# Performance work log

Measured on AMD Instinct MI355X. Metric: run time of the kernel, lower is better.

The kernel has to match this reference:

```python
import jax, jax.numpy as jnp
import numpy as np

N, E, R, D, L, B, K = 50000, 800000, 64, 64, 4, 2, 32


def setup_inputs() -> dict:
    ks = jax.random.split(jax.random.key(0), 10)
    return {
        "edge_index": jax.random.randint(ks[0], (2, E), 0, N),
        "edge_type": jax.random.randint(ks[1], (E,), 0, R),
        "h_index": jax.random.randint(ks[2], (B,), 0, N),
        "r_index": jax.random.randint(ks[3], (B,), 0, R),
        "t_index": jax.random.randint(ks[4], (B, K), 0, N),
        "rel_repr": jax.random.normal(ks[5], (B, R, D)) * 0.1,
        "boundary_extra": jax.random.normal(ks[6], (B, N, D)) * 0.02,
        "layers_W": jax.random.normal(ks[7], (L, 2 * D, D)) / np.sqrt(2 * D),
        "layers_b": jnp.zeros((L, D)),
        "ln_g": jnp.ones((L, D)),
        "ln_b": jnp.zeros((L, D)),
        "w1": jax.random.normal(ks[8], (2 * D, D)) / np.sqrt(2 * D),
        "b1": jnp.zeros((D,)),
        "w2": jax.random.normal(ks[9], (D,)) / np.sqrt(D),
        "b2": jnp.zeros((1,)),
    }


def _layer_norm(x, g, b, eps=1e-5):
    mu = x.mean(-1, keepdims=True)
    var = ((x - mu) ** 2).mean(-1, keepdims=True)
    return (x - mu) * jax.lax.rsqrt(var + eps) * g + b


def reference(edge_index, edge_type, h_index, r_index, t_index, rel_repr,
              boundary_extra, layers_W, layers_b, ln_g, ln_b, w1, b1, w2, b2):
    src, dst = edge_index[0], edge_index[1]
    query = rel_repr[jnp.arange(B), r_index]  # [B, D] per-query relation embedding
    # enhanced boundary: entity/relation-enhanced base + query injected at head node
    boundary = boundary_extra.at[jnp.arange(B), h_index].add(query)  # [B, N, D]
    seg = jax.vmap(lambda m: jax.ops.segment_sum(m, dst, num_segments=N))
    x = boundary
    for l in range(L):
        msg = x[:, src, :] * rel_repr[:, edge_type, :]   # DistMult messages [B, E, D]
        agg = seg(msg) + boundary                        # sum aggregation + boundary self-message
        out = jnp.einsum('bnd,df->bnf', jnp.concatenate([x, agg], -1), layers_W[l]) + layers_b[l]
        out = jax.nn.relu(_layer_norm(out, ln_g[l], ln_b[l]))
        x = out + x                                      # short_cut residual
    node_feat = jnp.concatenate(
        [x, jnp.broadcast_to(query[:, None, :], (B, N, D))], axis=-1)  # [B, N, 2D]
    feat = node_feat[jnp.arange(B)[:, None], t_index]    # gather tails [B, K, 2D]
    h = jax.nn.relu(feat @ w1 + b1)
    score = h @ w2 + b2                                  # [B, K]
    return score
```

## Files before the change

kernel.cpp:

```cpp
#include <hip/hip_runtime.h>
#include <hip/hip_bf16.h>

#define NN 50000
#define EE 800000
#define RR 64
#define DD 64
#define LL 4
#define BB 2
#define KK 32

#define NBUK 98
#define BROWS 512
#define CHUNK 2048
#define NBLK 391
#define PLACE_CAP 10240
#define CAP3 8192

#define PREP_BLKS 196
#define INIT_BLKS 3125
#define HIST_BLKS 391

#define PB_REL   0
#define PB_WT    8192
#define PB_LB    40960
#define PB_G     41216
#define PB_BETA  41472
#define PB_W1    41728
#define PB_B1    49920
#define PB_W2    49984
#define PB_B2    50048
#define PB_TOT   50049

typedef short v8s __attribute__((ext_vector_type(8)));
typedef float v4f __attribute__((ext_vector_type(4)));
typedef _Float16 v2h __attribute__((ext_vector_type(2)));
typedef _Float16 v4h __attribute__((ext_vector_type(4)));
typedef _Float16 v8h __attribute__((ext_vector_type(8)));
typedef unsigned short v4u __attribute__((ext_vector_type(4)));

static __device__ __forceinline__ float ldany(const void* p, int i, int flag) {
    if (flag) return __bfloat162float(((const __hip_bfloat16*)p)[i]);
    return ((const float*)p)[i];
}
static __device__ __forceinline__ unsigned short tobf(float x) {
    return (unsigned short)(__builtin_bit_cast(unsigned int, x) >> 16);
}
static __device__ __forceinline__ unsigned short rnebf(float x) {
    unsigned int u = __builtin_bit_cast(unsigned int, x);
    return (unsigned short)((u + 0x7FFFu + ((u >> 16) & 1u)) >> 16);
}
static __device__ __forceinline__ float frombf(unsigned short h) {
    return __builtin_bit_cast(float, ((unsigned int)h) << 16);
}
static __device__ __forceinline__ int getflag(const unsigned int* lng) {
    return (*lng == 0x3F803F80u) ? 1 : 0;
}

__global__ void __launch_bounds__(256) k_prep(const void* __restrict__ rel, const void* __restrict__ lb,
                       const void* __restrict__ g, const void* __restrict__ beta,
                       const void* __restrict__ w1, const void* __restrict__ b1,
                       const void* __restrict__ w2, const void* __restrict__ b2,
                       const void* __restrict__ W, const unsigned int* __restrict__ lng,
                       const void* __restrict__ be,
                       const int* __restrict__ h_index, const int* __restrict__ r_index,
                       const int* __restrict__ ei,
                       float* __restrict__ pb, unsigned short* __restrict__ wshi,
                       unsigned short* __restrict__ wslo, _Float16* __restrict__ relH,
                       _Float16* __restrict__ xH, int* __restrict__ bucketCount) {
    __shared__ int h[NBUK];
    int blk = blockIdx.x, t = threadIdx.x;
    int flag = getflag(lng);

    if (blk >= PREP_BLKS + INIT_BLKS) {
        if (t < NBUK) h[t] = 0;
        __syncthreads();
        int base = (blk - PREP_BLKS - INIT_BLKS) * CHUNK;
        #pragma unroll
        for (int i = 0; i < 8; ++i) {
            int e = base + i * 256 + t;
            if (e < EE) atomicAdd(&h[ei[EE + e] >> 9], 1);
        }
        __syncthreads();
        if (t < NBUK && h[t]) atomicAdd(&bucketCount[t], h[t]);
        return;
    }
    if (blk >= PREP_BLKS) {
        int gid = (blk - PREP_BLKS) * 256 + t;
        int n = gid >> 4, j = gid & 15, d0 = j * 4;
        float x0[4], x1[4];
        if (flag) {
            v4u a = *(const v4u*)((const unsigned short*)be + (size_t)n * 64 + d0);
            v4u bq = *(const v4u*)((const unsigned short*)be + (size_t)(NN + n) * 64 + d0);
            #pragma unroll
            for (int jj = 0; jj < 4; ++jj) { x0[jj] = frombf(a[jj]); x1[jj] = frombf(bq[jj]); }
        } else {
            v4f a = *(const v4f*)((const float*)be + (size_t)n * 64 + d0);
            v4f bq = *(const v4f*)((const float*)be + (size_t)(NN + n) * 64 + d0);
            #pragma unroll
            for (int jj = 0; jj < 4; ++jj) { x0[jj] = a[jj]; x1[jj] = bq[jj]; }
        }
        if (n == h_index[0]) {
            int r = r_index[0];
            #pragma unroll
            for (int jj = 0; jj < 4; ++jj) x0[jj] += ldany(rel, r * DD + d0 + jj, flag);
        }
        if (n == h_index[1]) {
            int r = r_index[1];
            #pragma unroll
            for (int jj = 0; jj < 4; ++jj) x1[jj] += ldany(rel, (RR + r) * DD + d0 + jj, flag);
        }
        v8h o;
        #pragma unroll
        for (int jj = 0; jj < 4; ++jj) {
            o[2 * jj]     = (_Float16)x0[jj];
            o[2 * jj + 1] = (_Float16)x1[jj];
        }
        *(v8h*)(xH + (size_t)n * 128 + d0 * 2) = o;
        return;
    }

    int gid = blk * 256 + t;
    if (gid < 32768) {
        int l = gid >> 13, r = gid & 8191, f = r >> 7, d = r & 127;
        float w = ldany(W, l * 8192 + d * 64 + f, flag);
        unsigned short h2 = tobf(w);
        wshi[gid] = h2;
        wslo[gid] = tobf(w - frombf(h2));
        if (gid < 8192) {
            int ty = gid >> 7, rr = gid & 127, dd = rr >> 1, b = rr & 1;
            relH[gid] = (_Float16)ldany(rel, b * 4096 + ty * 64 + dd, flag);
        }
    }
    if (gid >= PB_TOT) return;
    if (gid < PB_WT) { pb[gid] = ldany(rel, gid, flag); return; }
    if (gid < PB_LB) return;
    if (gid < PB_G)    { pb[gid] = ldany(lb,   gid - PB_LB,   flag); return; }
    if (gid < PB_BETA) { pb[gid] = ldany(g,    gid - PB_G,    flag); return; }
    if (gid < PB_W1)   { pb[gid] = ldany(beta, gid - PB_BETA, flag); return; }
    if (gid < PB_B1)   { pb[gid] = ldany(w1,   gid - PB_W1,   flag); return; }
    if (gid < PB_W2)   { pb[gid] = ldany(b1,   gid - PB_B1,   flag); return; }
    if (gid < PB_B2)   { pb[gid] = ldany(w2,   gid - PB_W2,   flag); return; }
    pb[gid] = ldany(b2, 0, flag);
}

__global__ void __launch_bounds__(256) k_bfill(const int* __restrict__ ei,
                                               const int* __restrict__ et,
                                               const int* __restrict__ bucketCount,
                                               int* __restrict__ bcur,
                                               unsigned int* __restrict__ btmp) {
    __shared__ int h[NBUK], rb[NBUK], sb[128];
    int t = threadIdx.x;
    int v = 0;
    if (t < 128) { v = (t < NBUK) ? bucketCount[t] : 0; sb[t] = v; }
    __syncthreads();
    for (int off = 1; off < 128; off <<= 1) {
        int a = (t < 128 && t >= off) ? sb[t - off] : 0;
        __syncthreads();
        if (t < 128 && t >= off) sb[t] += a;
        __syncthreads();
    }
    if (t < NBUK) sb[t] -= v;
    if (t < NBUK) h[t] = 0;
    __syncthreads();
    int base = blockIdx.x * CHUNK;
    unsigned int rec[8]; int bk[8];
    #pragma unroll
    for (int i = 0; i < 8; ++i) {
        int e = base + i * 256 + t;
        bk[i] = -1;
        if (e < EE) {
            int dst = ei[EE + e];
            rec[i] = (unsigned int)ei[e] | ((unsigned int)et[e] << 16)
                   | ((unsigned int)(dst & 511) << 22);
            bk[i] = dst >> 9;
            atomicAdd(&h[bk[i]], 1);
        }
    }
    __syncthreads();
    if (t < NBUK) rb[t] = h[t] ? (sb[t] + atomicAdd(&bcur[t], h[t])) : 0;
    __syncthreads();
    if (t < NBUK) h[t] = 0;
    __syncthreads();
    #pragma unroll
    for (int i = 0; i < 8; ++i) {
        if (bk[i] >= 0) {
            int pos = rb[bk[i]] + atomicAdd(&h[bk[i]], 1);
            btmp[pos] = rec[i];
        }
    }
}

__global__ void __launch_bounds__(256) k_place(const int* __restrict__ bucketCount,
                                               const unsigned int* __restrict__ btmp,
                                               unsigned int* __restrict__ elist,
                                               int* __restrict__ rowptr) {
    __shared__ int rp[BROWS + 1];
    __shared__ int cur[BROWS];
    __shared__ unsigned int outb[PLACE_CAP];
    __shared__ int sb[128];
    __shared__ int s_base, s_cnt;
    int b = blockIdx.x, t = threadIdx.x;
    int v = 0;
    if (t < 128) { v = (t < NBUK) ? bucketCount[t] : 0; sb[t] = v; }
    __syncthreads();
    for (int off = 1; off < 128; off <<= 1) {
        int a = (t < 128 && t >= off) ? sb[t - off] : 0;
        __syncthreads();
        if (t < 128 && t >= off) sb[t] += a;
        __syncthreads();
    }
    if (t == 0) { int cb = bucketCount[b]; s_base = sb[b] - cb; s_cnt = cb; }
    __syncthreads();
    int base = s_base;
    int cnt  = s_cnt;

    for (int r = t; r < BROWS; r += 256) cur[r] = 0;
    __syncthreads();
    for (int i = t; i < cnt; i += 256) {
        unsigned int rec = btmp[base + i];
        atomicAdd(&cur[rec >> 22], 1);
    }
    __syncthreads();
    if (t < 64) {
        int lane = t;
        int loc[8]; int s = 0;
        #pragma unroll
        for (int j = 0; j < 8; ++j) { loc[j] = s; s += cur[lane * 8 + j]; }
        int inc = s;
        for (int off = 1; off < 64; off <<= 1) {
            int vv = __shfl_up(inc, off, 64);
            if (lane >= off) inc += vv;
        }
        int excl = inc - s;
        #pragma unroll
        for (int j = 0; j < 8; ++j) rp[lane * 8 + j] = excl + loc[j];
        if (lane == 63) rp[BROWS] = inc;
    }
    __syncthreads();
    for (int r = t; r < BROWS; r += 256) cur[r] = rp[r];
    __syncthreads();
    for (int i = t; i < cnt; i += 256) {
        unsigned int rec = btmp[base + i];
        int ld = rec >> 22;
        int pos = atomicAdd(&cur[ld], 1);
        outb[pos] = rec & 0x3FFFFFu;
    }
    __syncthreads();
    for (int i = t; i < cnt; i += 256) elist[base + i] = outb[i];
    for (int r = t; r < BROWS; r += 256) {
        int n = b * BROWS + r;
        if (n <= NN) rowptr[n] = base + rp[r];
    }
}

__global__ void k_sets(const int* __restrict__ t_index,
                       const int* __restrict__ rowptr,
                       const unsigned int* __restrict__ elist,
                       int* __restrict__ flag3,
                       int* __restrict__ listT, int* __restrict__ posT,
                       int* __restrict__ list3, int* __restrict__ cnts) {
    __shared__ int sT, s3;
    __shared__ int lT[64];
    int t = threadIdx.x;
    if (t == 0) { sT = 0; s3 = 0; }
    __syncthreads();
    if (t < 64) {
        int n = t_index[t];
        if (atomicExch(&flag3[n], 1) == 0) {
            int p = atomicAdd(&sT, 1);
            lT[p] = n; listT[p] = n; list3[p] = n;
        }
    }
    __syncthreads();
    int nT = sT;
    if (t == 0) s3 = nT;
    __syncthreads();
    if (t < 64) {
        int n = t_index[t];
        int p = 0;
        for (int j = 0; j < nT; ++j) { if (lT[j] == n) { p = j; break; } }
        posT[t] = p;
    }
    int wave = t >> 6, lane = t & 63;
    for (int idx = wave; idx < nT; idx += 4) {
        int n = lT[idx];
        int s0 = rowptr[n], s1 = rowptr[n + 1];
        for (int i = s0 + lane; i < s1; i += 64) {
            int src = (int)(elist[i] & 0xFFFFu);
            if (atomicExch(&flag3[src], 1) == 0) {
                int p = atomicAdd(&s3, 1);
                if (p < CAP3) list3[p] = src;
            }
        }
    }
    __syncthreads();
    if (t == 0) { cnts[0] = nT; cnts[1] = (s3 > CAP3) ? CAP3 : s3; }
}

__global__ void __launch_bounds__(256) k_set2(const int* __restrict__ rowptr,
                                              const unsigned int* __restrict__ elist,
                                              const int* __restrict__ list3,
                                              const int* __restrict__ cnt3,
                                              int* __restrict__ flag2,
                                              int* __restrict__ list2,
                                              int* __restrict__ cnt2) {
    int wave = threadIdx.x >> 6, lane = threadIdx.x & 63;
    int nw = gridDim.x * 4;
    int c3 = *cnt3;
    for (int idx = blockIdx.x * 4 + wave; idx < c3; idx += nw) {
        int n = list3[idx];
        if (lane == 0) {
            if (atomicExch(&flag2[n], 1) == 0) list2[atomicAdd(cnt2, 1)] = n;
        }
        int s0 = rowptr[n], s1 = rowptr[n + 1];
        for (int i = s0 + lane; i < s1; i += 64) {
            int src = (int)(elist[i] & 0xFFFFu);
            if (atomicExch(&flag2[src], 1) == 0) {
                list2[atomicAdd(cnt2, 1)] = src;
            }
        }
    }
}

__global__ void __launch_bounds__(256) k_gather(const int* __restrict__ rowptr,
                                                const unsigned int* __restrict__ elist,
                                                const _Float16* __restrict__ xHin,
                                                const _Float16* __restrict__ relH,
                                                const void* __restrict__ be,
                                                const float* __restrict__ relf,
                                                const int* __restrict__ h_index,
                                                const int* __restrict__ r_index,
                                                const unsigned int* __restrict__ lng,
                                                const int* __restrict__ list,
                                                const int* __restrict__ cntp,
                                                unsigned short* __restrict__ aggH) {
    int wave = threadIdx.x >> 6, lane = threadIdx.x & 63;
    int idx = blockIdx.x * 4 + wave;
    int cnt = cntp ? *cntp : NN;
    if (idx >= cnt) return;
    int n = list ? list[idx] : idx;
    n = __builtin_amdgcn_readfirstlane(n);
    int start = __builtin_amdgcn_readfirstlane(rowptr[n]);
    int end   = __builtin_amdgcn_readfirstlane(rowptr[n + 1]);
    int flag  = getflag(lng);

    float a0 = ldany(be, n * DD + lane, flag);
    float a1 = ldany(be, (NN + n) * DD + lane, flag);
    if (n == h_index[0]) a0 += relf[(0 * RR + r_index[0]) * DD + lane];
    if (n == h_index[1]) a1 += relf[(1 * RR + r_index[1]) * DD + lane];

    for (int i = start; i < end; i += 8) {
        v2h xv[8], rv[8]; float mk[8];
        #pragma unroll
        for (int j = 0; j < 8; ++j) {
            int e = i + j;
            int ok = (e < end);
            unsigned int u = elist[ok ? e : start];
            int s = u & 0xFFFFu, ty = u >> 16;
            xv[j] = *(const v2h*)(xHin + s * 128 + lane * 2);
            rv[j] = *(const v2h*)(relH + ty * 128 + lane * 2);
            mk[j] = ok ? 1.f : 0.f;
        }
        #pragma unroll
        for (int j = 0; j < 8; ++j) {
            a0 += (float)xv[j].x * (float)rv[j].x * mk[j];
            a1 += (float)xv[j].y * (float)rv[j].y * mk[j];
        }
    }
    aggH[n * 64 + lane] = rnebf(a0);
    aggH[(NN + n) * 64 + lane] = rnebf(a1);
}

__global__ void __launch_bounds__(256) k_combine(const _Float16* __restrict__ xHin,
                                                 const unsigned short* __restrict__ aggH,
                                                 const unsigned short* __restrict__ whi,
                                                 const unsigned short* __restrict__ wlo,
                                                 const float* __restrict__ lb,
                                                 const float* __restrict__ g,
                                                 const float* __restrict__ beta,
                                                 const int* __restrict__ list,
                                                 const int* __restrict__ cntp,
                                                 _Float16* __restrict__ xHout) {
    __shared__ __attribute__((aligned(16))) unsigned short Xhi[64 * 136];
    __shared__ __attribute__((aligned(16))) unsigned short Xlo[64 * 72];
    __shared__ int nodes[32];
    float* outT = (float*)Xhi;

    int t = threadIdx.x;
    int cnt = cntp ? *cntp : NN;
    int ebase = blockIdx.x * 32;
    if (ebase >= cnt) return;

    if (t < 32) {
        int e = ebase + t;
        int ce = e < cnt ? e : cnt - 1;
        nodes[t] = list ? list[ce] : ce;
    }
    __syncthreads();

    #pragma unroll
    for (int it = 0; it < 4; ++it) {
        int idx = it * 256 + t;
        int nl = idx >> 5, j = idx & 31;
        int n = nodes[nl];
        v4h v = *(const v4h*)(xHin + (size_t)n * 128 + 4 * j);
        int r0 = nl, r1 = 32 + nl;
        int k0 = 2 * j, k1 = 2 * j + 1;
        float f; unsigned short h;
        f = (float)v.x; h = tobf(f); Xhi[r0 * 136 + k0] = h; Xlo[r0 * 72 + k0] = tobf(f - frombf(h));
        f = (float)v.y; h = tobf(f); Xhi[r1 * 136 + k0] = h; Xlo[r1 * 72 + k0] = tobf(f - frombf(h));
        f = (float)v.z; h = tobf(f); Xhi[r0 * 136 + k1] = h; Xlo[r0 * 72 + k1] = tobf(f - frombf(h));
        f = (float)v.w; h = tobf(f); Xhi[r1 * 136 + k1] = h; Xlo[r1 * 72 + k1] = tobf(f - frombf(h));
    }
    #pragma unroll
    for (int it = 0; it < 4; ++it) {
        int idx = it * 256 + t;
        int half = idx >> 9, rem = idx & 511;
        int nl = rem >> 4, j = rem & 15;
        int n = nodes[nl];
        v4u v = *(const v4u*)(aggH + (size_t)(half * NN + n) * 64 + 4 * j);
        int row = half * 32 + nl;
        int kb = 64 + 4 * j;
        Xhi[row * 136 + kb + 0] = v.x;
        Xhi[row * 136 + kb + 1] = v.y;
        Xhi[row * 136 + kb + 2] = v.z;
        Xhi[row * 136 + kb + 3] = v.w;
    }
    __syncthreads();

    int wave = t >> 6, lane = t & 63;
    int low = lane & 15, q = lane >> 4;

    v4f acc[4];
    #pragma unroll
    for (int ft = 0; ft < 4; ++ft) acc[ft] = 0.f;

    int arow = wave * 16 + low;
    #pragma unroll
    for (int kt = 0; kt < 2; ++kt) {
        int k0 = kt * 32 + q * 8;
        v8s ah = *(const v8s*)(Xhi + arow * 136 + k0);
        v8s al = *(const v8s*)(Xlo + arow * 72 + k0);
        #pragma unroll
        for (int ft = 0; ft < 4; ++ft) {
            v8s bh = *(const v8s*)(whi + (ft * 16 + low) * 128 + k0);
            v8s bl = *(const v8s*)(wlo + (ft * 16 + low) * 128 + k0);
            acc[ft] = __builtin_amdgcn_mfma_f32_16x16x32_bf16(ah, bh, acc[ft], 0, 0, 0);
            acc[ft] = __builtin_amdgcn_mfma_f32_16x16x32_bf16(al, bh, acc[ft], 0, 0, 0);
            acc[ft] = __builtin_amdgcn_mfma_f32_16x16x32_bf16(ah, bl, acc[ft], 0, 0, 0);
        }
    }
    #pragma unroll
    for (int kt = 2; kt < 4; ++kt) {
        int k0 = kt * 32 + q * 8;
        v8s ah = *(const v8s*)(Xhi + arow * 136 + k0);
        #pragma unroll
        for (int ft = 0; ft < 4; ++ft) {
            v8s bh = *(const v8s*)(whi + (ft * 16 + low) * 128 + k0);
            v8s bl = *(const v8s*)(wlo + (ft * 16 + low) * 128 + k0);
            acc[ft] = __builtin_amdgcn_mfma_f32_16x16x32_bf16(ah, bh, acc[ft], 0, 0, 0);
            acc[ft] = __builtin_amdgcn_mfma_f32_16x16x32_bf16(ah, bl, acc[ft], 0, 0, 0);
        }
    }

    float o[4][4];
    #pragma unroll
    for (int ft = 0; ft < 4; ++ft) {
        float lbv = lb[ft * 16 + low];
        #pragma unroll
        for (int r = 0; r < 4; ++r) o[ft][r] = acc[ft][r] + lbv;
    }
    float s1[4], s2[4];
    #pragma unroll
    for (int r = 0; r < 4; ++r) {
        s1[r] = o[0][r] + o[1][r] + o[2][r] + o[3][r];
        s2[r] = o[0][r]*o[0][r] + o[1][r]*o[1][r] + o[2][r]*o[2][r] + o[3][r]*o[3][r];
    }
    #pragma unroll
    for (int m = 1; m < 16; m <<= 1) {
        #pragma unroll
        for (int r = 0; r < 4; ++r) {
            s1[r] += __shfl_xor(s1[r], m, 64);
            s2[r] += __shfl_xor(s2[r], m, 64);
        }
    }
    float res[4][4];
    #pragma unroll
    for (int r = 0; r < 4; ++r) {
        int row = wave * 16 + q * 4 + r;
        float mu  = s1[r] * (1.f / 64.f);
        float var = s2[r] * (1.f / 64.f) - mu * mu;
        float rs  = rsqrtf(fmaxf(var, 0.f) + 1e-5f);
        #pragma unroll
        for (int ft = 0; ft < 4; ++ft) {
            int f = ft * 16 + low;
            float xold = frombf(Xhi[row * 136 + f]) + frombf(Xlo[row * 72 + f]);
            res[ft][r] = fmaxf((o[ft][r] - mu) * rs * g[f] + beta[f], 0.f) + xold;
        }
    }
    __syncthreads();

    #pragma unroll
    for (int r = 0; r < 4; ++r) {
        int row = wave * 16 + q * 4 + r;
        #pragma unroll
        for (int ft = 0; ft < 4; ++ft) outT[row * 65 + ft * 16 + low] = res[ft][r];
    }
    __syncthreads();

    #pragma unroll
    for (int it = 0; it < 4; ++it) {
        int idx = it * 256 + t;
        int nl = idx >> 5, j = idx & 31;
        if (ebase + nl < cnt) {
            int n = nodes[nl];
            v4h hv;
            hv.x = (_Float16)outT[nl * 65 + 2 * j];
            hv.y = (_Float16)outT[(32 + nl) * 65 + 2 * j];
            hv.z = (_Float16)outT[nl * 65 + 2 * j + 1];
            hv.w = (_Float16)outT[(32 + nl) * 65 + 2 * j + 1];
            *(v4h*)(xHout + (size_t)n * 128 + 4 * j) = hv;
        }
    }
}

template<int FINAL>
__global__ void __launch_bounds__(256) k_gc(const int* __restrict__ rowptr,
                                            const unsigned int* __restrict__ elist,
                                            const _Float16* __restrict__ xHin,
                                            const _Float16* __restrict__ relH,
                                            const void* __restrict__ be,
                                            const float* __restrict__ pb,
                                            const int* __restrict__ h_index,
                                            const int* __restrict__ r_index,
                                            const unsigned int* __restrict__ lng,
                                            const int* __restrict__ list,
                                            const int* __restrict__ cntp,
                                            const unsigned short* __restrict__ whi,
                                            const unsigned short* __restrict__ wlo,
                                            const float* __restrict__ lb,
                                            const float* __restrict__ g,
                                            const float* __restrict__ beta,
                                            _Float16* __restrict__ xHout,
                                            const int* __restrict__ posT,
                                            void* __restrict__ out) {
    __shared__ float xrow[8][64];
    __shared__ float aggL[8][64];
    __shared__ float resL[8][64];
    int t = threadIdx.x, wave = t >> 6, lane = t & 63;
    int cnt = *cntp;
    int ebase = blockIdx.x * 4;
    if (ebase >= cnt) return;
    int idx = ebase + wave;
    int flag = getflag(lng);
    const float* relf = pb + PB_REL;
    int active = (idx < cnt);

    int n = -1;
    float xa = 0.f, xb = 0.f, a0 = 0.f, a1 = 0.f;
    if (active) {
        n = __builtin_amdgcn_readfirstlane(list[idx]);
        int start = __builtin_amdgcn_readfirstlane(rowptr[n]);
        int end   = __builtin_amdgcn_readfirstlane(rowptr[n + 1]);
        v2h xv2 = *(const v2h*)(xHin + (size_t)n * 128 + lane * 2);
        xa = (float)xv2.x; xb = (float)xv2.y;
        a0 = ldany(be, n * DD + lane, flag);
        a1 = ldany(be, (NN + n) * DD + lane, flag);
        if (n == h_index[0]) a0 += relf[(0 * RR + r_index[0]) * DD + lane];
        if (n == h_index[1]) a1 += relf[(1 * RR + r_index[1]) * DD + lane];
        for (int i = start; i < end; i += 8) {
            v2h xv[8], rv[8]; float mk[8];
            #pragma unroll
            for (int j = 0; j < 8; ++j) {
                int e = i + j;
                int ok = (e < end);
                unsigned int u = elist[ok ? e : start];
                int s = u & 0xFFFFu, ty = u >> 16;
                xv[j] = *(const v2h*)(xHin + s * 128 + lane * 2);
                rv[j] = *(const v2h*)(relH + ty * 128 + lane * 2);
                mk[j] = ok ? 1.f : 0.f;
            }
            #pragma unroll
            for (int j = 0; j < 8; ++j) {
                a0 += (float)xv[j].x * (float)rv[j].x * mk[j];
                a1 += (float)xv[j].y * (float)rv[j].y * mk[j];
            }
        }
        a0 = frombf(rnebf(a0));
        a1 = frombf(rnebf(a1));
    }
    xrow[wave * 2 + 0][lane] = xa;
    xrow[wave * 2 + 1][lane] = xb;
    aggL[wave * 2 + 0][lane] = a0;
    aggL[wave * 2 + 1][lane] = a1;
    __syncthreads();

    int f = lane;
    int r0 = wave * 2, r1 = wave * 2 + 1;
    float d0 = lb[f], d1 = d0;
    for (int k0 = 0; k0 < 64; k0 += 8) {
        v8s wh = *(const v8s*)(whi + f * 128 + k0);
        v8s wl = *(const v8s*)(wlo + f * 128 + k0);
        #pragma unroll
        for (int j = 0; j < 8; ++j) {
            float wv = frombf((unsigned short)wh[j]) + frombf((unsigned short)wl[j]);
            d0 += xrow[r0][k0 + j] * wv;
            d1 += xrow[r1][k0 + j] * wv;
        }
    }
    for (int k0 = 64; k0 < 128; k0 += 8) {
        v8s wh = *(const v8s*)(whi + f * 128 + k0);
        v8s wl = *(const v8s*)(wlo + f * 128 + k0);
        #pragma unroll
        for (int j = 0; j < 8; ++j) {
            float wv = frombf((unsigned short)wh[j]) + frombf((unsigned short)wl[j]);
            d0 += aggL[r0][k0 + j - 64] * wv;
            d1 += aggL[r1][k0 + j - 64] * wv;
        }
    }
    float s1a = d0, s2a = d0 * d0, s1b = d1, s2b = d1 * d1;
    #pragma unroll
    for (int m = 1; m < 64; m <<= 1) {
        s1a += __shfl_xor(s1a, m, 64);
        s2a += __shfl_xor(s2a, m, 64);
        s1b += __shfl_xor(s1b, m, 64);
        s2b += __shfl_xor(s2b, m, 64);
    }
    float mua = s1a * (1.f / 64.f);
    float vara = s2a * (1.f / 64.f) - mua * mua;
    float rsa = rsqrtf(fmaxf(vara, 0.f) + 1e-5f);
    float mub = s1b * (1.f / 64.f);
    float varb = s2b * (1.f / 64.f) - mub * mub;
    float rsb = rsqrtf(fmaxf(varb, 0.f) + 1e-5f);
    float gv = g[f], bv = beta[f];
    float res0 = fmaxf((d0 - mua) * rsa * gv + bv, 0.f) + xa;
    float res1 = fmaxf((d1 - mub) * rsb * gv + bv, 0.f) + xb;

    if (active) {
        v2h hv; hv.x = (_Float16)res0; hv.y = (_Float16)res1;
        *(v2h*)(xHout + (size_t)n * 128 + lane * 2) = hv;
    }

    if (FINAL) {
        resL[r0][lane] = res0;
        resL[r1][lane] = res1;
        __syncthreads();
        const float* w1 = pb + PB_W1;
        for (int j = wave; j < BB * KK; j += 4) {
            int pj = posT[j];
            if (pj >= ebase && pj < ebase + 4) {
                int b = j >> 5, k = j & 31;
                int row = (pj - ebase) * 2 + b;
                const float* qv = relf + (b * RR + r_index[b]) * DD;
                float acc2 = pb[PB_B1 + lane];
                #pragma unroll 8
                for (int d = 0; d < 64; ++d) acc2 += resL[row][d] * w1[d * 64 + lane];
                #pragma unroll 8
                for (int d = 0; d < 64; ++d) acc2 += qv[d] * w1[(64 + d) * 64 + lane];
                float hh = fmaxf(acc2, 0.f);
                float p = hh * pb[PB_W2 + lane];
                for (int m = 32; m > 0; m >>= 1) p += __shfl_xor(p, m, 64);
                if (lane == 0) {
                    float s = p + pb[PB_B2];
                    if (flag) ((__hip_bfloat16*)out)[b * KK + k] = __float2bfloat16(s);
                    else      ((float*)out)[b * KK + k] = s;
                }
            }
        }
    }
}

extern "C" void kernel_launch(void* const* d_in, const int* in_sizes, int n_in,
                              void* d_out, int out_size, void* d_ws, size_t ws_size,
                              hipStream_t stream) {
    const int* edge_index = (const int*)d_in[0];
    const int* edge_type  = (const int*)d_in[1];
    const int* h_index    = (const int*)d_in[2];
    const int* r_index    = (const int*)d_in[3];
    const int* t_index    = (const int*)d_in[4];
    const void* rel   = d_in[5];
    const void* be    = d_in[6];
    const void* lw    = d_in[7];
    const void* lbias = d_in[8];
    const void* lng   = d_in[9];
    const void* lnb   = d_in[10];
    const void* w1    = d_in[11];
    const void* b1    = d_in[12];
    const void* w2    = d_in[13];
    const void* b2    = d_in[14];

    _Float16* xHa = (_Float16*)d_ws;
    _Float16* xHb = xHa + (size_t)NN * 128;
    unsigned short* aggH = (unsigned short*)(xHb + (size_t)NN * 128);
    float*    pb  = (float*)(aggH + (size_t)BB * NN * 64);
    int*      ip  = (int*)(pb + PB_TOT);
    int* bucketCount = ip;
    int* bcur   = bucketCount + NBUK;
    int* flag2  = bcur + NBUK;
    int* flag3  = flag2 + NN;
    int* cnts   = flag3 + NN;
    int* rowptr = cnts + 16;
    int* listT  = rowptr + NN + 1;
    int* posT   = listT + 64;
    int* list3  = posT + 64;
    int* list2  = list3 + CAP3;
    unsigned int* elist = (unsigned int*)(list2 + NN);
    unsigned short* wshi = (unsigned short*)(elist + EE);
    unsigned short* wslo = wshi + 32768;
    _Float16* relH = (_Float16*)(wslo + 32768);
    unsigned int* btmp = (unsigned int*)xHb;
    const unsigned int* lngp = (const unsigned int*)lng;

    hipMemsetAsync(bucketCount, 0, (size_t)(2 * NBUK + 2 * NN + 16) * sizeof(int), stream);
    k_prep<<<PREP_BLKS + INIT_BLKS + HIST_BLKS, 256, 0, stream>>>(
        rel, lbias, lng, lnb, w1, b1, w2, b2, lw, lngp, be, h_index, r_index,
        edge_index, pb, wshi, wslo, relH, xHa, bucketCount);
    k_bfill<<<NBLK, 256, 0, stream>>>(edge_index, edge_type, bucketCount, bcur, btmp);
    k_place<<<NBUK, 256, 0, stream>>>(bucketCount, btmp, elist, rowptr);
    k_sets<<<1, 256, 0, stream>>>(t_index, rowptr, elist, flag3, listT, posT, list3, cnts);
    k_set2<<<256, 256, 0, stream>>>(rowptr, elist, list3, cnts + 1, flag2, list2, cnts + 2);

    const float* relf = pb + PB_REL;
    k_gather<<<12500, 256, 0, stream>>>(rowptr, elist, xHa, relH, be, relf,
                                        h_index, r_index, lngp, nullptr, nullptr, aggH);
    k_combine<<<1563, 256, 0, stream>>>(xHa, aggH, wshi + 0, wslo + 0,
                                        pb + PB_LB + 0, pb + PB_G + 0, pb + PB_BETA + 0,
                                        nullptr, nullptr, xHb);
    k_gather<<<12500, 256, 0, stream>>>(rowptr, elist, xHb, relH, be, relf,
                                        h_index, r_index, lngp, list2, cnts + 2, aggH);
    k_combine<<<1563, 256, 0, stream>>>(xHb, aggH, wshi + 8192, wslo + 8192,
                                        pb + PB_LB + 64, pb + PB_G + 64, pb + PB_BETA + 64,
                                        list2, cnts + 2, xHa);
    k_gc<0><<<2048, 256, 0, stream>>>(rowptr, elist, xHa, relH, be, pb,
                                      h_index, r_index, lngp, list3, cnts + 1,
                                      wshi + 16384, wslo + 16384,
                                      pb + PB_LB + 128, pb + PB_G + 128, pb + PB_BETA + 128,
                                      xHb, nullptr, nullptr);
    k_gc<1><<<16, 256, 0, stream>>>(rowptr, elist, xHb, relH, be, pb,
                                    h_index, r_index, lngp, listT, cnts + 0,
                                    wshi + 24576, wslo + 24576,
                                    pb + PB_LB + 192, pb + PB_G + 192, pb + PB_BETA + 192,
                                    xHa, posT, d_out);
}
```

Measured before the change: 336.1 us.

## Fuse gather and combine into one per-layer kernel with fp32 LDS weights

Drops the separate gather and MFMA combine kernels for the first two layers and uses the fused gather+combine kernel for every layer, so the bf16 aggregate buffer no longer goes through global memory. Weights are kept in fp32 and staged in LDS per block (32 KB), replacing the split-bf16 hi/lo MFMA scheme. The dense 128x64 matvec now uses wave shuffles and scalar FMAs in place of matrix cores. Blocks grow to 512 threads handling 8 nodes each. This saves a kernel launch and an intermediate round trip per layer, but it moves the dense math onto the vector ALUs and reloads the full weight matrix into LDS for every block.

```diff
diff --git a/kernel.cpp b/kernel.cpp
--- a/kernel.cpp
+++ b/kernel.cpp
@@ -31,19 +31,14 @@
 #define PB_B2    50048
 #define PB_TOT   50049
 
-typedef short v8s __attribute__((ext_vector_type(8)));
 typedef float v4f __attribute__((ext_vector_type(4)));
 typedef _Float16 v2h __attribute__((ext_vector_type(2)));
-typedef _Float16 v4h __attribute__((ext_vector_type(4)));
 typedef _Float16 v8h __attribute__((ext_vector_type(8)));
 typedef unsigned short v4u __attribute__((ext_vector_type(4)));
 
 static __device__ __forceinline__ float ldany(const void* p, int i, int flag) {
     if (flag) return __bfloat162float(((const __hip_bfloat16*)p)[i]);
     return ((const float*)p)[i];
-}
-static __device__ __forceinline__ unsigned short tobf(float x) {
-    return (unsigned short)(__builtin_bit_cast(unsigned int, x) >> 16);
 }
 static __device__ __forceinline__ unsigned short rnebf(float x) {
     unsigned int u = __builtin_bit_cast(unsigned int, x);
@@ -64,8 +59,7 @@
                        const void* __restrict__ be,
                        const int* __restrict__ h_index, const int* __restrict__ r_index,
                        const int* __restrict__ ei,
-                       float* __restrict__ pb, unsigned short* __restrict__ wshi,
-                       unsigned short* __restrict__ wslo, _Float16* __restrict__ relH,
+                       float* __restrict__ pb, _Float16* __restrict__ relH,
                        _Float16* __restrict__ xH, int* __restrict__ bucketCount) {
     __shared__ int h[NBUK];
     int blk = blockIdx.x, t = threadIdx.x;
@@ -121,11 +115,7 @@
 
     int gid = blk * 256 + t;
     if (gid < 32768) {
-        int l = gid >> 13, r = gid & 8191, f = r >> 7, d = r & 127;
-        float w = ldany(W, l * 8192 + d * 64 + f, flag);
-        unsigned short h2 = tobf(w);
-        wshi[gid] = h2;
-        wslo[gid] = tobf(w - frombf(h2));
+        pb[PB_WT + gid] = ldany(W, gid, flag);
         if (gid < 8192) {
             int ty = gid >> 7, rr = gid & 127, dd = rr >> 1, b = rr & 1;
             relH[gid] = (_Float16)ldany(rel, b * 4096 + ty * 64 + dd, flag);
@@ -322,210 +312,8 @@
     }
 }
 
-__global__ void __launch_bounds__(256) k_gather(const int* __restrict__ rowptr,
-                                                const unsigned int* __restrict__ elist,
-                                                const _Float16* __restrict__ xHin,
-                                                const _Float16* __restrict__ relH,
-                                                const void* __restrict__ be,
-                                                const float* __restrict__ relf,
-                                                const int* __restrict__ h_index,
-                                                const int* __restrict__ r_index,
-                                                const unsigned int* __restrict__ lng,
-                                                const int* __restrict__ list,
-                                                const int* __restrict__ cntp,
-                                                unsigned short* __restrict__ aggH) {
-    int wave = threadIdx.x >> 6, lane = threadIdx.x & 63;
-    int idx = blockIdx.x * 4 + wave;
-    int cnt = cntp ? *cntp : NN;
-    if (idx >= cnt) return;
-    int n = list ? list[idx] : idx;
-    n = __builtin_amdgcn_readfirstlane(n);
-    int start = __builtin_amdgcn_readfirstlane(rowptr[n]);
-    int end   = __builtin_amdgcn_readfirstlane(rowptr[n + 1]);
-    int flag  = getflag(lng);
-
-    float a0 = ldany(be, n * DD + lane, flag);
-    float a1 = ldany(be, (NN + n) * DD + lane, flag);
-    if (n == h_index[0]) a0 += relf[(0 * RR + r_index[0]) * DD + lane];
-    if (n == h_index[1]) a1 += relf[(1 * RR + r_index[1]) * DD + lane];
-
-    for (int i = start; i < end; i += 8) {
-        v2h xv[8], rv[8]; float mk[8];
-        #pragma unroll
-        for (int j = 0; j < 8; ++j) {
-            int e = i + j;
-            int ok = (e < end);
-            unsigned int u = elist[ok ? e : start];
-            int s = u & 0xFFFFu, ty = u >> 16;
-            xv[j] = *(const v2h*)(xHin + s * 128 + lane * 2);
-            rv[j] = *(const v2h*)(relH + ty * 128 + lane * 2);
-            mk[j] = ok ? 1.f : 0.f;
-        }
-        #pragma unroll
-        for (int j = 0; j < 8; ++j) {
-            a0 += (float)xv[j].x * (float)rv[j].x * mk[j];
-            a1 += (float)xv[j].y * (float)rv[j].y * mk[j];
-        }
-    }
-    aggH[n * 64 + lane] = rnebf(a0);
-    aggH[(NN + n) * 64 + lane] = rnebf(a1);
-}
-
-__global__ void __launch_bounds__(256) k_combine(const _Float16* __restrict__ xHin,
-                                                 const unsigned short* __restrict__ aggH,
-                                                 const unsigned short* __restrict__ whi,
-                                                 const unsigned short* __restrict__ wlo,
-                                                 const float* __restrict__ lb,
-                                                 const float* __restrict__ g,
-                                                 const float* __restrict__ beta,
-                                                 const int* __restrict__ list,
-                                                 const int* __restrict__ cntp,
-                                                 _Float16* __restrict__ xHout) {
-    __shared__ __attribute__((aligned(16))) unsigned short Xhi[64 * 136];
-    __shared__ __attribute__((aligned(16))) unsigned short Xlo[64 * 72];
-    __shared__ int nodes[32];
-    float* outT = (float*)Xhi;
-
-    int t = threadIdx.x;
-    int cnt = cntp ? *cntp : NN;
-    int ebase = blockIdx.x * 32;
-    if (ebase >= cnt) return;
-
-    if (t < 32) {
-        int e = ebase + t;
-        int ce = e < cnt ? e : cnt - 1;
-        nodes[t] = list ? list[ce] : ce;
-    }
-    __syncthreads();
-
-    #pragma unroll
-    for (int it = 0; it < 4; ++it) {
-        int idx = it * 256 + t;
-        int nl = idx >> 5, j = idx & 31;
-        int n = nodes[nl];
-        v4h v = *(const v4h*)(xHin + (size_t)n * 128 + 4 * j);
-        int r0 = nl, r1 = 32 + nl;
-        int k0 = 2 * j, k1 = 2 * j + 1;
-        float f; unsigned short h;
-        f = (float)v.x; h = tobf(f); Xhi[r0 * 136 + k0] = h; Xlo[r0 * 72 + k0] = tobf(f - frombf(h));
-        f = (float)v.y; h = tobf(f); Xhi[r1 * 136 + k0] = h; Xlo[r1 * 72 + k0] = tobf(f - frombf(h));
-        f = (float)v.z; h = tobf(f); Xhi[r0 * 136 + k1] = h; Xlo[r0 * 72 + k1] = tobf(f - frombf(h));
-        f = (float)v.w; h = tobf(f); Xhi[r1 * 136 + k1] = h; Xlo[r1 * 72 + k1] = tobf(f - frombf(h));
-    }
-    #pragma unroll
-    for (int it = 0; it < 4; ++it) {
-        int idx = it * 256 + t;
-        int half = idx >> 9, rem = idx & 511;
-        int nl = rem >> 4, j = rem & 15;
-        int n = nodes[nl];
-        v4u v = *(const v4u*)(aggH + (size_t)(half * NN + n) * 64 + 4 * j);
-        int row = half * 32 + nl;
-        int kb = 64 + 4 * j;
-        Xhi[row * 136 + kb + 0] = v.x;
-        Xhi[row * 136 + kb + 1] = v.y;
-        Xhi[row * 136 + kb + 2] = v.z;
-        Xhi[row * 136 + kb + 3] = v.w;
-    }
-    __syncthreads();
-
-    int wave = t >> 6, lane = t & 63;
-    int low = lane & 15, q = lane >> 4;
-
-    v4f acc[4];
-    #pragma unroll
-    for (int ft = 0; ft < 4; ++ft) acc[ft] = 0.f;
-
-    int arow = wave * 16 + low;
-    #pragma unroll
-    for (int kt = 0; kt < 2; ++kt) {
-        int k0 = kt * 32 + q * 8;
-        v8s ah = *(const v8s*)(Xhi + arow * 136 + k0);
-        v8s al = *(const v8s*)(Xlo + arow * 72 + k0);
-        #pragma unroll
-        for (int ft = 0; ft < 4; ++ft) {
-            v8s bh = *(const v8s*)(whi + (ft * 16 + low) * 128 + k0);
-            v8s bl = *(const v8s*)(wlo + (ft * 16 + low) * 128 + k0);
-            acc[ft] = __builtin_amdgcn_mfma_f32_16x16x32_bf16(ah, bh, acc[ft], 0, 0, 0);
-            acc[ft] = __builtin_amdgcn_mfma_f32_16x16x32_bf16(al, bh, acc[ft], 0, 0, 0);
-            acc[ft] = __builtin_amdgcn_mfma_f32_16x16x32_bf16(ah, bl, acc[ft], 0, 0, 0);
-        }
-    }
-    #pragma unroll
-    for (int kt = 2; kt < 4; ++kt) {
-        int k0 = kt * 32 + q * 8;
-        v8s ah = *(const v8s*)(Xhi + arow * 136 + k0);
-        #pragma unroll
-        for (int ft = 0; ft < 4; ++ft) {
-            v8s bh = *(const v8s*)(whi + (ft * 16 + low) * 128 + k0);
-            v8s bl = *(const v8s*)(wlo + (ft * 16 + low) * 128 + k0);
-            acc[ft] = __builtin_amdgcn_mfma_f32_16x16x32_bf16(ah, bh, acc[ft], 0, 0, 0);
-            acc[ft] = __builtin_amdgcn_mfma_f32_16x16x32_bf16(ah, bl, acc[ft], 0, 0, 0);
-        }
-    }
-
-    float o[4][4];
-    #pragma unroll
-    for (int ft = 0; ft < 4; ++ft) {
-        float lbv = lb[ft * 16 + low];
-        #pragma unroll
-        for (int r = 0; r < 4; ++r) o[ft][r] = acc[ft][r] + lbv;
-    }
-    float s1[4], s2[4];
-    #pragma unroll
-    for (int r = 0; r < 4; ++r) {
-        s1[r] = o[0][r] + o[1][r] + o[2][r] + o[3][r];
-        s2[r] = o[0][r]*o[0][r] + o[1][r]*o[1][r] + o[2][r]*o[2][r] + o[3][r]*o[3][r];
-    }
-    #pragma unroll
-    for (int m = 1; m < 16; m <<= 1) {
-        #pragma unroll
-        for (int r = 0; r < 4; ++r) {
-            s1[r] += __shfl_xor(s1[r], m, 64);
-            s2[r] += __shfl_xor(s2[r], m, 64);
-        }
-    }
-    float res[4][4];
-    #pragma unroll
-    for (int r = 0; r < 4; ++r) {
-        int row = wave * 16 + q * 4 + r;
-        float mu  = s1[r] * (1.f / 64.f);
-        float var = s2[r] * (1.f / 64.f) - mu * mu;
-        float rs  = rsqrtf(fmaxf(var, 0.f) + 1e-5f);
-        #pragma unroll
-        for (int ft = 0; ft < 4; ++ft) {
-            int f = ft * 16 + low;
-            float xold = frombf(Xhi[row * 136 + f]) + frombf(Xlo[row * 72 + f]);
-            res[ft][r] = fmaxf((o[ft][r] - mu) * rs * g[f] + beta[f], 0.f) + xold;
-        }
-    }
-    __syncthreads();
-
-    #pragma unroll
-    for (int r = 0; r < 4; ++r) {
-        int row = wave * 16 + q * 4 + r;
-        #pragma unroll
-        for (int ft = 0; ft < 4; ++ft) outT[row * 65 + ft * 16 + low] = res[ft][r];
-    }
-    __syncthreads();
-
-    #pragma unroll
-    for (int it = 0; it < 4; ++it) {
-        int idx = it * 256 + t;
-        int nl = idx >> 5, j = idx & 31;
-        if (ebase + nl < cnt) {
-            int n = nodes[nl];
-            v4h hv;
-            hv.x = (_Float16)outT[nl * 65 + 2 * j];
-            hv.y = (_Float16)outT[(32 + nl) * 65 + 2 * j];
-            hv.z = (_Float16)outT[nl * 65 + 2 * j + 1];
-            hv.w = (_Float16)outT[(32 + nl) * 65 + 2 * j + 1];
-            *(v4h*)(xHout + (size_t)n * 128 + 4 * j) = hv;
-        }
-    }
-}
-
 template<int FINAL>
-__global__ void __launch_bounds__(256) k_gc(const int* __restrict__ rowptr,
+__global__ void __launch_bounds__(512) k_gc(const int* __restrict__ rowptr,
                                             const unsigned int* __restrict__ elist,
                                             const _Float16* __restrict__ xHin,
                                             const _Float16* __restrict__ relH,
@@ -536,30 +324,33 @@
                                             const unsigned int* __restrict__ lng,
                                             const int* __restrict__ list,
                                             const int* __restrict__ cntp,
-                                            const unsigned short* __restrict__ whi,
-                                            const unsigned short* __restrict__ wlo,
+                                            const float* __restrict__ wsrc,
                                             const float* __restrict__ lb,
                                             const float* __restrict__ g,
                                             const float* __restrict__ beta,
                                             _Float16* __restrict__ xHout,
                                             const int* __restrict__ posT,
                                             void* __restrict__ out) {
-    __shared__ float xrow[8][64];
-    __shared__ float aggL[8][64];
-    __shared__ float resL[8][64];
+    __shared__ float wf[8192];
     int t = threadIdx.x, wave = t >> 6, lane = t & 63;
-    int cnt = *cntp;
-    int ebase = blockIdx.x * 4;
+    int cnt = cntp ? *cntp : NN;
+    int ebase = blockIdx.x * 8;
     if (ebase >= cnt) return;
+
+    #pragma unroll
+    for (int j = 0; j < 4; ++j)
+        ((v4f*)wf)[t + j * 512] = ((const v4f*)wsrc)[t + j * 512];
+    __syncthreads();
+
     int idx = ebase + wave;
     int flag = getflag(lng);
     const float* relf = pb + PB_REL;
     int active = (idx < cnt);
 
-    int n = -1;
+    int n = 0;
     float xa = 0.f, xb = 0.f, a0 = 0.f, a1 = 0.f;
     if (active) {
-        n = __builtin_amdgcn_readfirstlane(list[idx]);
+        n = __builtin_amdgcn_readfirstlane(list ? list[idx] : idx);
         int start = __builtin_amdgcn_readfirstlane(rowptr[n]);
         int end   = __builtin_amdgcn_readfirstlane(rowptr[n + 1]);
         v2h xv2 = *(const v2h*)(xHin + (size_t)n * 128 + lane * 2);
@@ -589,34 +380,20 @@
         a0 = frombf(rnebf(a0));
         a1 = frombf(rnebf(a1));
     }
-    xrow[wave * 2 + 0][lane] = xa;
-    xrow[wave * 2 + 1][lane] = xb;
-    aggL[wave * 2 + 0][lane] = a0;
-    aggL[wave * 2 + 1][lane] = a1;
-    __syncthreads();
 
     int f = lane;
-    int r0 = wave * 2, r1 = wave * 2 + 1;
     float d0 = lb[f], d1 = d0;
-    for (int k0 = 0; k0 < 64; k0 += 8) {
-        v8s wh = *(const v8s*)(whi + f * 128 + k0);
-        v8s wl = *(const v8s*)(wlo + f * 128 + k0);
-        #pragma unroll
-        for (int j = 0; j < 8; ++j) {
-            float wv = frombf((unsigned short)wh[j]) + frombf((unsigned short)wl[j]);
-            d0 += xrow[r0][k0 + j] * wv;
-            d1 += xrow[r1][k0 + j] * wv;
-        }
-    }
-    for (int k0 = 64; k0 < 128; k0 += 8) {
-        v8s wh = *(const v8s*)(whi + f * 128 + k0);
-        v8s wl = *(const v8s*)(wlo + f * 128 + k0);
-        #pragma unroll
-        for (int j = 0; j < 8; ++j) {
-            float wv = frombf((unsigned short)wh[j]) + frombf((unsigned short)wl[j]);
-            d0 += aggL[r0][k0 + j - 64] * wv;
-            d1 += aggL[r1][k0 + j - 64] * wv;
-        }
+    #pragma unroll
+    for (int k = 0; k < 64; ++k) {
+        float wv = wf[k * 64 + f];
+        d0 += __shfl(xa, k, 64) * wv;
+        d1 += __shfl(xb, k, 64) * wv;
+    }
+    #pragma unroll
+    for (int k = 0; k < 64; ++k) {
+        float wv = wf[(64 + k) * 64 + f];
+        d0 += __shfl(a0, k, 64) * wv;
+        d1 += __shfl(a1, k, 64) * wv;
     }
     float s1a = d0, s2a = d0 * d0, s1b = d1, s2b = d1 * d1;
     #pragma unroll
@@ -632,9 +409,8 @@
     float mub = s1b * (1.f / 64.f);
     float varb = s2b * (1.f / 64.f) - mub * mub;
     float rsb = rsqrtf(fmaxf(varb, 0.f) + 1e-5f);
-    float gv = g[f], bv = beta[f];
-    float res0 = fmaxf((d0 - mua) * rsa * gv + bv, 0.f) + xa;
-    float res1 = fmaxf((d1 - mub) * rsb * gv + bv, 0.f) + xb;
+    float res0 = fmaxf((d0 - mua) * rsa * g[f] + beta[f], 0.f) + xa;
+    float res1 = fmaxf((d1 - mub) * rsb * g[f] + beta[f], 0.f) + xb;
 
     if (active) {
         v2h hv; hv.x = (_Float16)res0; hv.y = (_Float16)res1;
@@ -642,28 +418,27 @@
     }
 
     if (FINAL) {
-        resL[r0][lane] = res0;
-        resL[r1][lane] = res1;
-        __syncthreads();
-        const float* w1 = pb + PB_W1;
-        for (int j = wave; j < BB * KK; j += 4) {
-            int pj = posT[j];
-            if (pj >= ebase && pj < ebase + 4) {
-                int b = j >> 5, k = j & 31;
-                int row = (pj - ebase) * 2 + b;
-                const float* qv = relf + (b * RR + r_index[b]) * DD;
-                float acc2 = pb[PB_B1 + lane];
-                #pragma unroll 8
-                for (int d = 0; d < 64; ++d) acc2 += resL[row][d] * w1[d * 64 + lane];
-                #pragma unroll 8
-                for (int d = 0; d < 64; ++d) acc2 += qv[d] * w1[(64 + d) * 64 + lane];
-                float hh = fmaxf(acc2, 0.f);
-                float p = hh * pb[PB_W2 + lane];
-                for (int m = 32; m > 0; m >>= 1) p += __shfl_xor(p, m, 64);
-                if (lane == 0) {
-                    float s = p + pb[PB_B2];
-                    if (flag) ((__hip_bfloat16*)out)[b * KK + k] = __float2bfloat16(s);
-                    else      ((float*)out)[b * KK + k] = s;
+        if (active) {
+            const float* w1 = pb + PB_W1;
+            for (int j = 0; j < BB * KK; ++j) {
+                if (posT[j] == idx) {
+                    int b = j >> 5, k = j & 31;
+                    float rv = b ? res1 : res0;
+                    const float* qv = relf + (b * RR + r_index[b]) * DD;
+                    float acc2 = pb[PB_B1 + lane];
+                    #pragma unroll
+                    for (int d = 0; d < 64; ++d) {
+                        acc2 += __shfl(rv, d, 64) * w1[d * 64 + lane];
+                        acc2 += qv[d] * w1[(64 + d) * 64 + lane];
+                    }
+                    float hh = fmaxf(acc2, 0.f);
+                    float p = hh * pb[PB_W2 + lane];
+                    for (int m = 32; m > 0; m >>= 1) p += __shfl_xor(p, m, 64);
+                    if (lane == 0) {
+                        float s = p + pb[PB_B2];
+                        if (flag) ((__hip_bfloat16*)out)[b * KK + k] = __float2bfloat16(s);
+                        else      ((float*)out)[b * KK + k] = s;
+                    }
                 }
             }
         }
@@ -691,8 +466,7 @@
 
     _Float16* xHa = (_Float16*)d_ws;
     _Float16* xHb = xHa + (size_t)NN * 128;
-    unsigned short* aggH = (unsigned short*)(xHb + (size_t)NN * 128);
-    float*    pb  = (float*)(aggH + (size_t)BB * NN * 64);
+    float*    pb  = (float*)(xHb + (size_t)NN * 128);
     int*      ip  = (int*)(pb + PB_TOT);
     int* bucketCount = ip;
     int* bcur   = bucketCount + NBUK;
@@ -705,40 +479,34 @@
     int* list3  = posT + 64;
     int* list2  = list3 + CAP3;
     unsigned int* elist = (unsigned int*)(list2 + NN);
-    unsigned short* wshi = (unsigned short*)(elist + EE);
-    unsigned short* wslo = wshi + 32768;
-    _Float16* relH = (_Float16*)(wslo + 32768);
+    _Float16* relH = (_Float16*)(elist + EE);
     unsigned int* btmp = (unsigned int*)xHb;
     const unsigned int* lngp = (const unsigned int*)lng;
 
     hipMemsetAsync(bucketCount, 0, (size_t)(2 * NBUK + 2 * NN + 16) * sizeof(int), stream);
     k_prep<<<PREP_BLKS + INIT_BLKS + HIST_BLKS, 256, 0, stream>>>(
         rel, lbias, lng, lnb, w1, b1, w2, b2, lw, lngp, be, h_index, r_index,
-        edge_index, pb, wshi, wslo, relH, xHa, bucketCount);
+        edge_index, pb, relH, xHa, bucketCount);
     k_bfill<<<NBLK, 256, 0, stream>>>(edge_index, edge_type, bucketCount, bcur, btmp);
     k_place<<<NBUK, 256, 0, stream>>>(bucketCount, btmp, elist, rowptr);
     k_sets<<<1, 256, 0, stream>>>(t_index, rowptr, elist, flag3, listT, posT, list3, cnts);
     k_set2<<<256, 256, 0, stream>>>(rowptr, elist, list3, cnts + 1, flag2, list2, cnts + 2);
 
-    const float* relf = pb + PB_REL;
-    k_gather<<<12500, 256, 0, stream>>>(rowptr, elist, xHa, relH, be, relf,
-                                        h_index, r_index, lngp, nullptr, nullptr, aggH);
-    k_combine<<<1563, 256, 0, stream>>>(xHa, aggH, wshi + 0, wslo + 0,
-                                        pb + PB_LB + 0, pb + PB_G + 0, pb + PB_BETA + 0,
-                                        nullptr, nullptr, xHb);
-    k_gather<<<12500, 256, 0, stream>>>(rowptr, elist, xHb, relH, be, relf,
-                                        h_index, r_index, lngp, list2, cnts + 2, aggH);
-    k_combine<<<1563, 256, 0, stream>>>(xHb, aggH, wshi + 8192, wslo + 8192,
-                                        pb + PB_LB + 64, pb + PB_G + 64, pb + PB_BETA + 64,
-                                        list2, cnts + 2, xHa);
-    k_gc<0><<<2048, 256, 0, stream>>>(rowptr, elist, xHa, relH, be, pb,
+    const float* wt = pb + PB_WT;
+    k_gc<0><<<6250, 512, 0, stream>>>(rowptr, elist, xHa, relH, be, pb,
+                                      h_index, r_index, lngp, nullptr, nullptr,
+                                      wt + 0, pb + PB_LB + 0, pb + PB_G + 0,
+                                      pb + PB_BETA + 0, xHb, nullptr, nullptr);
+    k_gc<0><<<6250, 512, 0, stream>>>(rowptr, elist, xHb, relH, be, pb,
+                                      h_index, r_index, lngp, list2, cnts + 2,
+                                      wt + 8192, pb + PB_LB + 64, pb + PB_G + 64,
+                                      pb + PB_BETA + 64, xHa, nullptr, nullptr);
+    k_gc<0><<<1024, 512, 0, stream>>>(rowptr, elist, xHa, relH, be, pb,
                                       h_index, r_index, lngp, list3, cnts + 1,
-                                      wshi + 16384, wslo + 16384,
-                                      pb + PB_LB + 128, pb + PB_G + 128, pb + PB_BETA + 128,
-                                      xHb, nullptr, nullptr);
-    k_gc<1><<<16, 256, 0, stream>>>(rowptr, elist, xHb, relH, be, pb,
-                                    h_index, r_index, lngp, listT, cnts + 0,
-                                    wshi + 24576, wslo + 24576,
-                                    pb + PB_LB + 192, pb + PB_G + 192, pb + PB_BETA + 192,
-                                    xHa, posT, d_out);
-}
+                                      wt + 16384, pb + PB_LB + 128, pb + PB_G + 128,
+                                      pb + PB_BETA + 128, xHb, nullptr, nullptr);
+    k_gc<1><<<8, 512, 0, stream>>>(rowptr, elist, xHb, relH, be, pb,
+                                   h_index, r_index, lngp, listT, cnts + 0,
+                                   wt + 24576, pb + PB_LB + 192, pb + PB_G + 192,
+                                   pb + PB_BETA + 192, xHa, posT, d_out);
+}
```

After: 485.3 us. 44.4% more time.
